# Performance work log

Measured on AMD Instinct MI355X. Metric: run time of the kernel, lower is better.

## Reference

```python
import jax, jax.numpy as jnp
import numpy as np
import math


def _attn(q, k, v):
    # q,k,v: [B, S, d] (d == 1 here). bmm -> scale -> softmax -> bmm.
    scale = 1.0 / math.sqrt(q.shape[2])
    e = jnp.einsum('bsd,btd->bst', q, k) * scale  # [B, S, S]
    w = jax.nn.softmax(e, axis=2)
    return jnp.einsum('bst,btd->bsd', w, v)


def setup_inputs() -> dict:
    key = jax.random.key(0)
    ks = jax.random.split(key, 12)
    B, D = 32, 768
    CLF_OUT = 7
    inp = {}
    names = ['sentence', 'target_spkr_snts', 'other_spkr_snts', 'scene_desc', 'scene_sent']
    for i, name in enumerate(names):
        inp[name] = jax.random.normal(ks[i], (B, D), dtype=jnp.float32)
    inp['W_shared'] = jax.random.normal(ks[5], (768, 512), dtype=jnp.float32) * 0.02
    inp['b_shared'] = jnp.zeros((512,), dtype=jnp.float32)
    inp['W1'] = jax.random.normal(ks[6], (3840, 256), dtype=jnp.float32) * 0.02
    inp['b1'] = jnp.zeros((256,), dtype=jnp.float32)
    inp['W2'] = jax.random.normal(ks[7], (256, CLF_OUT), dtype=jnp.float32) * 0.02
    inp['b2'] = jnp.zeros((CLF_OUT,), dtype=jnp.float32)
    return inp


def reference(sentence, target_spkr_snts, other_spkr_snts, scene_desc, scene_sent,
              W_shared, b_shared, W1, b1, W2, b2):
    B = sentence.shape[0]
    s = sentence[..., None]             # [B, 768, 1]
    sd = scene_desc[..., None]
    ts = target_spkr_snts[..., None]
    oth = other_spkr_snts[..., None]
    ss = scene_sent[..., None]

    speaker_context = _attn(oth, ts, ts)   # [B, 768, 1]
    scene_context = _attn(ss, ss, sd)      # [B, 768, 1]

    sentence_shared = sentence @ W_shared + b_shared                     # [B, 512]
    scene_context_shared = scene_context.reshape(B, -1) @ W_shared + b_shared
    speaker_context_shared = speaker_context.reshape(B, -1) @ W_shared + b_shared

    fused = jnp.concatenate([s, scene_context, speaker_context], axis=1)  # [B, 2304, 1]
    z = _attn(fused, fused, fused)                                        # [B, 2304, 1]

    final = jnp.concatenate([z.reshape(B, -1), sentence_shared,
                             scene_context_shared, speaker_context_shared], axis=1)  # [B, 3840]
    h = jax.nn.relu(final @ W1 + b1)   # dropout is identity in eval mode
    return jax.nn.sigmoid(h @ W2 + b2)  # [B, 7]
```

## Files before the change

### kernel.cpp

```cpp
#include <hip/hip_runtime.h>
#include <math.h>

#define LOG2E 1.44269504088896340736f
typedef float v2f __attribute__((ext_vector_type(2)));


__device__ __forceinline__ void proj_512(
    const float* __restrict__ xsrc,
    const float* __restrict__ Ws,
    const float* __restrict__ bs,
    float* __restrict__ dst,
    float* xb,
    float (*red)[512],
    int tid)
{
    if (tid < 512) { xb[tid] = xsrc[tid]; }
    if (tid >= 256) { xb[tid + 256] = xsrc[tid + 256]; }
    __syncthreads();

    const int g = tid >> 7;
    const int q = tid & 127;
    const float4* __restrict__ Wv = (const float4*)Ws;
    float ax = 0.f, ay = 0.f, az = 0.f, aw = 0.f;
    #pragma unroll 8
    for (int k = g; k < 768; k += 4) {
        const float xv = xb[k];
        const float4 w = Wv[k * 128 + q];
        ax += xv * w.x; ay += xv * w.y; az += xv * w.z; aw += xv * w.w;
    }
    red[g][q * 4 + 0] = ax;
    red[g][q * 4 + 1] = ay;
    red[g][q * 4 + 2] = az;
    red[g][q * 4 + 3] = aw;
    __syncthreads();

    if (tid < 512) {
        dst[tid] = bs[tid] + red[0][tid] + red[1][tid] + red[2][tid] + red[3][tid];
    }
}

__global__ __launch_bounds__(512) void k1_small_attn_proj0(
    const float* __restrict__ sentence,
    const float* __restrict__ target,
    const float* __restrict__ other,
    const float* __restrict__ scene_desc,
    const float* __restrict__ scene_sent,
    const float* __restrict__ Ws,
    const float* __restrict__ bs,
    float* __restrict__ ctx,
    float* __restrict__ final_)
{
    const int b = blockIdx.x;
    const int y = blockIdx.y;
    const int tid = threadIdx.x;
    __shared__ float s0[768];
    __shared__ float s1[768];
    __shared__ float red[4][512];

    if (y < 12) {
        const int part = y / 6;
        const int rg = y - part * 6;
        const float* qp; const float* kp; const float* vp;
        if (part == 0) { qp = scene_sent + b * 768; kp = qp;               vp = scene_desc + b * 768; }
        else           { qp = other + b * 768;      kp = target + b * 768; vp = kp; }
        for (int i = tid; i < 768; i += 512) { s0[i] = kp[i]; s1[i] = vp[i]; }
        __syncthreads();

        const int r0  = rg * 128 + (tid >> 3);
        const int r1  = r0 + 64;
        const int sub = tid & 7;
        const float qA = qp[r0] * LOG2E;
        const float qB = qp[r1] * LOG2E;
        const v2f qA2 = {qA, qA}, qB2 = {qB, qB};
        const float4* __restrict__ kv = (const float4*)s0;
        const float4* __restrict__ vv = (const float4*)s1;
        v2f nA0 = {0.f,0.f}, nA1 = {0.f,0.f}, dA0 = {0.f,0.f}, dA1 = {0.f,0.f};
        v2f nB0 = {0.f,0.f}, nB1 = {0.f,0.f}, dB0 = {0.f,0.f}, dB1 = {0.f,0.f};
        #pragma unroll 4
        for (int i = 0; i < 24; ++i) {
            const int j = sub + 8 * i;
            const float4 k4 = kv[j];
            const float4 v4 = vv[j];
            const v2f ka = {k4.x, k4.y}, kb = {k4.z, k4.w};
            const v2f va = {v4.x, v4.y}, vb2 = {v4.z, v4.w};
            const v2f xaA = qA2 * ka, xbA = qA2 * kb;
            const v2f eaA = {__builtin_amdgcn_exp2f(xaA.x), __builtin_amdgcn_exp2f(xaA.y)};
            const v2f ebA = {__builtin_amdgcn_exp2f(xbA.x), __builtin_amdgcn_exp2f(xbA.y)};
            nA0 += eaA * va;  dA0 += eaA;
            nA1 += ebA * vb2; dA1 += ebA;
            const v2f xaB = qB2 * ka, xbB = qB2 * kb;
            const v2f eaB = {__builtin_amdgcn_exp2f(xaB.x), __builtin_amdgcn_exp2f(xaB.y)};
            const v2f ebB = {__builtin_amdgcn_exp2f(xbB.x), __builtin_amdgcn_exp2f(xbB.y)};
            nB0 += eaB * va;  dB0 += eaB;
            nB1 += ebB * vb2; dB1 += ebB;
        }
        float numA = (nA0.x + nA0.y) + (nA1.x + nA1.y);
        float denA = (dA0.x + dA0.y) + (dA1.x + dA1.y);
        float numB = (nB0.x + nB0.y) + (nB1.x + nB1.y);
        float denB = (dB0.x + dB0.y) + (dB1.x + dB1.y);
        numA += __shfl_xor(numA, 1, 64); numA += __shfl_xor(numA, 2, 64); numA += __shfl_xor(numA, 4, 64);
        denA += __shfl_xor(denA, 1, 64); denA += __shfl_xor(denA, 2, 64); denA += __shfl_xor(denA, 4, 64);
        numB += __shfl_xor(numB, 1, 64); numB += __shfl_xor(numB, 2, 64); numB += __shfl_xor(numB, 4, 64);
        denB += __shfl_xor(denB, 1, 64); denB += __shfl_xor(denB, 2, 64); denB += __shfl_xor(denB, 4, 64);
        if (sub == 0) {
            ctx[b * 1536 + part * 768 + r0] = numA / denA;
            ctx[b * 1536 + part * 768 + r1] = numB / denB;
        }
    } else {
        proj_512(sentence + b * 768, Ws, bs, final_ + b * 3840 + 2304, s0, red, tid);
    }
}

__global__ __launch_bounds__(512) void k2_fused_attn_proj12(
    const float* __restrict__ sentence,
    const float* __restrict__ ctx,
    const float* __restrict__ Ws,
    const float* __restrict__ bs,
    float* __restrict__ final_)
{
    const int b = blockIdx.x;
    const int y = blockIdx.y;
    const int tid = threadIdx.x;
    __shared__ float vb[2304];
    __shared__ float red[4][512];

    if (y < 18) {
        for (int i = tid; i < 2304; i += 512)
            vb[i] = (i < 768) ? sentence[b * 768 + i] : ctx[b * 1536 + (i - 768)];
        __syncthreads();

        const int r0  = y * 128 + (tid >> 3);
        const int r1  = r0 + 64;
        const int sub = tid & 7;
        const float qA = vb[r0] * LOG2E;
        const float qB = vb[r1] * LOG2E;
        const v2f qA2 = {qA, qA}, qB2 = {qB, qB};
        const float4* __restrict__ fv = (const float4*)vb;
        v2f nA0 = {0.f,0.f}, nA1 = {0.f,0.f}, dA0 = {0.f,0.f}, dA1 = {0.f,0.f};
        v2f nB0 = {0.f,0.f}, nB1 = {0.f,0.f}, dB0 = {0.f,0.f}, dB1 = {0.f,0.f};
        #pragma unroll 4
        for (int i = 0; i < 72; ++i) {
            const int j = sub + 8 * i;
            const float4 f4 = fv[j];
            const v2f fa = {f4.x, f4.y}, fb = {f4.z, f4.w};
            const v2f xaA = qA2 * fa, xbA = qA2 * fb;
            const v2f eaA = {__builtin_amdgcn_exp2f(xaA.x), __builtin_amdgcn_exp2f(xaA.y)};
            const v2f ebA = {__builtin_amdgcn_exp2f(xbA.x), __builtin_amdgcn_exp2f(xbA.y)};
            nA0 += eaA * fa; dA0 += eaA;
            nA1 += ebA * fb; dA1 += ebA;
            const v2f xaB = qB2 * fa, xbB = qB2 * fb;
            const v2f eaB = {__builtin_amdgcn_exp2f(xaB.x), __builtin_amdgcn_exp2f(xaB.y)};
            const v2f ebB = {__builtin_amdgcn_exp2f(xbB.x), __builtin_amdgcn_exp2f(xbB.y)};
            nB0 += eaB * fa; dB0 += eaB;
            nB1 += ebB * fb; dB1 += ebB;
        }
        float numA = (nA0.x + nA0.y) + (nA1.x + nA1.y);
        float denA = (dA0.x + dA0.y) + (dA1.x + dA1.y);
        float numB = (nB0.x + nB0.y) + (nB1.x + nB1.y);
        float denB = (dB0.x + dB0.y) + (dB1.x + dB1.y);
        numA += __shfl_xor(numA, 1, 64); numA += __shfl_xor(numA, 2, 64); numA += __shfl_xor(numA, 4, 64);
        denA += __shfl_xor(denA, 1, 64); denA += __shfl_xor(denA, 2, 64); denA += __shfl_xor(denA, 4, 64);
        numB += __shfl_xor(numB, 1, 64); numB += __shfl_xor(numB, 2, 64); numB += __shfl_xor(numB, 4, 64);
        denB += __shfl_xor(denB, 1, 64); denB += __shfl_xor(denB, 2, 64); denB += __shfl_xor(denB, 4, 64);
        if (sub == 0) {
            final_[b * 3840 + r0] = numA / denA;
            final_[b * 3840 + r1] = numB / denB;
        }
    } else {
        const int p = y - 17;
        proj_512(ctx + b * 1536 + (p - 1) * 768, Ws, bs,
                 final_ + b * 3840 + 2304 + p * 512, vb, red, tid);
    }
}

__global__ __launch_bounds__(1024) void mlp_part_kernel(
    const float* __restrict__ final_,
    const float* __restrict__ W1,
    float* __restrict__ hpart)
{
    const int b = blockIdx.x;
    const int c = blockIdx.y;
    const int tid = threadIdx.x;
    const int base = c * 480;

    __shared__ float fb[480];
    __shared__ float red[16][256];
    if (tid < 480) fb[tid] = final_[b * 3840 + base + tid];
    __syncthreads();

    const int g = tid >> 6;
    const int q = tid & 63;
    const float4* __restrict__ Wv = (const float4*)W1;
    float ax = 0.f, ay = 0.f, az = 0.f, aw = 0.f;
    const int l0 = g * 30;
    #pragma unroll 5
    for (int kk = 0; kk < 30; ++kk) {
        const float xv = fb[l0 + kk];
        const float4 w = Wv[(base + l0 + kk) * 64 + q];
        ax += xv * w.x; ay += xv * w.y; az += xv * w.z; aw += xv * w.w;
    }
    red[g][q * 4 + 0] = ax;
    red[g][q * 4 + 1] = ay;
    red[g][q * 4 + 2] = az;
    red[g][q * 4 + 3] = aw;
    __syncthreads();

    if (tid < 256) {
        float s = 0.f;
        #pragma unroll
        for (int g2 = 0; g2 < 16; ++g2) s += red[g2][tid];
        hpart[(b * 8 + c) * 256 + tid] = s;
    }
}

__global__ __launch_bounds__(512) void mlp_tail_kernel(
    const float* __restrict__ hpart,
    const float* __restrict__ b1,
    const float* __restrict__ W2,
    const float* __restrict__ b2,
    float* __restrict__ out)
{
    const int b = blockIdx.x;
    const int tid = threadIdx.x;

    __shared__ float hb[256];
    if (tid < 256) {
        float s = b1[tid];
        #pragma unroll
        for (int c = 0; c < 8; ++c) s += hpart[(b * 8 + c) * 256 + tid];
        hb[tid] = fmaxf(s, 0.f);
    }
    __syncthreads();

    const int w = tid >> 6;
    const int lane = tid & 63;
    if (w < 7) {
        float a = 0.f;
        #pragma unroll
        for (int c = lane; c < 256; c += 64)
            a += hb[c] * W2[c * 7 + w];
        #pragma unroll
        for (int off = 32; off > 0; off >>= 1)
            a += __shfl_down(a, off, 64);
        if (lane == 0)
            out[b * 7 + w] = 1.f / (1.f + __expf(-(a + b2[w])));
    }
}

extern "C" void kernel_launch(void* const* d_in, const int* in_sizes, int n_in,
                              void* d_out, int out_size, void* d_ws, size_t ws_size,
                              hipStream_t stream) {
    const float* sentence   = (const float*)d_in[0];
    const float* target     = (const float*)d_in[1];
    const float* other      = (const float*)d_in[2];
    const float* scene_desc = (const float*)d_in[3];
    const float* scene_sent = (const float*)d_in[4];
    const float* Ws         = (const float*)d_in[5];
    const float* bs         = (const float*)d_in[6];
    const float* W1         = (const float*)d_in[7];
    const float* b1         = (const float*)d_in[8];
    const float* W2         = (const float*)d_in[9];
    const float* b2         = (const float*)d_in[10];
    float* out = (float*)d_out;

    float* ctx    = (float*)d_ws;
    float* final_ = ctx + 32 * 1536;
    float* hpart  = final_ + 32 * 3840;

    k1_small_attn_proj0<<<dim3(32, 13), 512, 0, stream>>>(sentence, target, other,
                                                          scene_desc, scene_sent,
                                                          Ws, bs, ctx, final_);
    k2_fused_attn_proj12<<<dim3(32, 20), 512, 0, stream>>>(sentence, ctx, Ws, bs, final_);
    mlp_part_kernel<<<dim3(32, 8), 1024, 0, stream>>>(final_, W1, hpart);
    mlp_tail_kernel<<<32, 512, 0, stream>>>(hpart, b1, W2, b2, out);
}
```

Baseline: 58.22 us.

## Merge four kernels into one cooperative persistent kernel with grid syncs

Replaces the four separate launches (small attention plus projection, fused attention plus projections, MLP partial, MLP tail) with a single cooperative kernel. Blocks loop over work items per phase and use grid.sync between phases. The MLP partial stage is also split into 16 chunks of 240 rows instead of 8 of 480. This targets launch overhead and inter-kernel gaps, but adds grid-wide barrier cost and an occupancy query on the host every call.

New measurement: 164.8 us. 183% more time.

```diff
diff --git a/kernel.cpp b/kernel.cpp
--- a/kernel.cpp
+++ b/kernel.cpp
@@ -1,17 +1,20 @@
 #include <hip/hip_runtime.h>
+#include <hip/hip_cooperative_groups.h>
 #include <math.h>
+
+namespace cg = cooperative_groups;
 
 #define LOG2E 1.44269504088896340736f
 typedef float v2f __attribute__((ext_vector_type(2)));
 
 
-__device__ __forceinline__ void proj_512(
+__device__ __forceinline__ void proj_768x512(
     const float* __restrict__ xsrc,
     const float* __restrict__ Ws,
     const float* __restrict__ bs,
     float* __restrict__ dst,
     float* xb,
-    float (*red)[512],
+    float* redf,
     int tid)
 {
     if (tid < 512) { xb[tid] = xsrc[tid]; }
@@ -28,18 +31,67 @@
         const float4 w = Wv[k * 128 + q];
         ax += xv * w.x; ay += xv * w.y; az += xv * w.z; aw += xv * w.w;
     }
-    red[g][q * 4 + 0] = ax;
-    red[g][q * 4 + 1] = ay;
-    red[g][q * 4 + 2] = az;
-    red[g][q * 4 + 3] = aw;
+    redf[g * 512 + q * 4 + 0] = ax;
+    redf[g * 512 + q * 4 + 1] = ay;
+    redf[g * 512 + q * 4 + 2] = az;
+    redf[g * 512 + q * 4 + 3] = aw;
     __syncthreads();
 
     if (tid < 512) {
-        dst[tid] = bs[tid] + red[0][tid] + red[1][tid] + red[2][tid] + red[3][tid];
-    }
-}
-
-__global__ __launch_bounds__(512) void k1_small_attn_proj0(
+        dst[tid] = bs[tid] + redf[0 * 512 + tid] + redf[1 * 512 + tid]
+                           + redf[2 * 512 + tid] + redf[3 * 512 + tid];
+    }
+}
+
+__device__ __forceinline__ void attn128(
+    const float* __restrict__ qsrc,
+    const float4* __restrict__ kv,
+    const float4* __restrict__ vv,
+    int n4,
+    int r0base, int tid,
+    float* __restrict__ out0,
+    int outstride_r0)
+{
+    const int r0  = r0base + (tid >> 3);
+    const int r1  = r0 + 64;
+    const int sub = tid & 7;
+    const float qA = qsrc[r0] * LOG2E;
+    const float qB = qsrc[r1] * LOG2E;
+    const v2f qA2 = {qA, qA}, qB2 = {qB, qB};
+    v2f nA0 = {0.f,0.f}, nA1 = {0.f,0.f}, dA0 = {0.f,0.f}, dA1 = {0.f,0.f};
+    v2f nB0 = {0.f,0.f}, nB1 = {0.f,0.f}, dB0 = {0.f,0.f}, dB1 = {0.f,0.f};
+    #pragma unroll 4
+    for (int j = sub; j < n4; j += 8) {
+        const float4 k4 = kv[j];
+        const float4 v4 = vv[j];
+        const v2f ka = {k4.x, k4.y}, kb = {k4.z, k4.w};
+        const v2f va = {v4.x, v4.y}, vb2 = {v4.z, v4.w};
+        const v2f xaA = qA2 * ka, xbA = qA2 * kb;
+        const v2f eaA = {__builtin_amdgcn_exp2f(xaA.x), __builtin_amdgcn_exp2f(xaA.y)};
+        const v2f ebA = {__builtin_amdgcn_exp2f(xbA.x), __builtin_amdgcn_exp2f(xbA.y)};
+        nA0 += eaA * va;  dA0 += eaA;
+        nA1 += ebA * vb2; dA1 += ebA;
+        const v2f xaB = qB2 * ka, xbB = qB2 * kb;
+        const v2f eaB = {__builtin_amdgcn_exp2f(xaB.x), __builtin_amdgcn_exp2f(xaB.y)};
+        const v2f ebB = {__builtin_amdgcn_exp2f(xbB.x), __builtin_amdgcn_exp2f(xbB.y)};
+        nB0 += eaB * va;  dB0 += eaB;
+        nB1 += ebB * vb2; dB1 += ebB;
+    }
+    float numA = (nA0.x + nA0.y) + (nA1.x + nA1.y);
+    float denA = (dA0.x + dA0.y) + (dA1.x + dA1.y);
+    float numB = (nB0.x + nB0.y) + (nB1.x + nB1.y);
+    float denB = (dB0.x + dB0.y) + (dB1.x + dB1.y);
+    numA += __shfl_xor(numA, 1, 64); numA += __shfl_xor(numA, 2, 64); numA += __shfl_xor(numA, 4, 64);
+    denA += __shfl_xor(denA, 1, 64); denA += __shfl_xor(denA, 2, 64); denA += __shfl_xor(denA, 4, 64);
+    numB += __shfl_xor(numB, 1, 64); numB += __shfl_xor(numB, 2, 64); numB += __shfl_xor(numB, 4, 64);
+    denB += __shfl_xor(denB, 1, 64); denB += __shfl_xor(denB, 2, 64); denB += __shfl_xor(denB, 4, 64);
+    if (sub == 0) {
+        out0[outstride_r0 + r0 - r0base] = numA / denA;
+        out0[outstride_r0 + r1 - r0base] = numB / denB;
+    }
+}
+
+__global__ __launch_bounds__(512) void mega_kernel(
     const float* __restrict__ sentence,
     const float* __restrict__ target,
     const float* __restrict__ other,
@@ -47,203 +99,120 @@
     const float* __restrict__ scene_sent,
     const float* __restrict__ Ws,
     const float* __restrict__ bs,
-    float* __restrict__ ctx,
-    float* __restrict__ final_)
-{
-    const int b = blockIdx.x;
-    const int y = blockIdx.y;
-    const int tid = threadIdx.x;
-    __shared__ float s0[768];
-    __shared__ float s1[768];
-    __shared__ float red[4][512];
-
-    if (y < 12) {
-        const int part = y / 6;
-        const int rg = y - part * 6;
-        const float* qp; const float* kp; const float* vp;
-        if (part == 0) { qp = scene_sent + b * 768; kp = qp;               vp = scene_desc + b * 768; }
-        else           { qp = other + b * 768;      kp = target + b * 768; vp = kp; }
-        for (int i = tid; i < 768; i += 512) { s0[i] = kp[i]; s1[i] = vp[i]; }
-        __syncthreads();
-
-        const int r0  = rg * 128 + (tid >> 3);
-        const int r1  = r0 + 64;
-        const int sub = tid & 7;
-        const float qA = qp[r0] * LOG2E;
-        const float qB = qp[r1] * LOG2E;
-        const v2f qA2 = {qA, qA}, qB2 = {qB, qB};
-        const float4* __restrict__ kv = (const float4*)s0;
-        const float4* __restrict__ vv = (const float4*)s1;
-        v2f nA0 = {0.f,0.f}, nA1 = {0.f,0.f}, dA0 = {0.f,0.f}, dA1 = {0.f,0.f};
-        v2f nB0 = {0.f,0.f}, nB1 = {0.f,0.f}, dB0 = {0.f,0.f}, dB1 = {0.f,0.f};
-        #pragma unroll 4
-        for (int i = 0; i < 24; ++i) {
-            const int j = sub + 8 * i;
-            const float4 k4 = kv[j];
-            const float4 v4 = vv[j];
-            const v2f ka = {k4.x, k4.y}, kb = {k4.z, k4.w};
-            const v2f va = {v4.x, v4.y}, vb2 = {v4.z, v4.w};
-            const v2f xaA = qA2 * ka, xbA = qA2 * kb;
-            const v2f eaA = {__builtin_amdgcn_exp2f(xaA.x), __builtin_amdgcn_exp2f(xaA.y)};
-            const v2f ebA = {__builtin_amdgcn_exp2f(xbA.x), __builtin_amdgcn_exp2f(xbA.y)};
-            nA0 += eaA * va;  dA0 += eaA;
-            nA1 += ebA * vb2; dA1 += ebA;
-            const v2f xaB = qB2 * ka, xbB = qB2 * kb;
-            const v2f eaB = {__builtin_amdgcn_exp2f(xaB.x), __builtin_amdgcn_exp2f(xaB.y)};
-            const v2f ebB = {__builtin_amdgcn_exp2f(xbB.x), __builtin_amdgcn_exp2f(xbB.y)};
-            nB0 += eaB * va;  dB0 += eaB;
-            nB1 += ebB * vb2; dB1 += ebB;
-        }
-        float numA = (nA0.x + nA0.y) + (nA1.x + nA1.y);
-        float denA = (dA0.x + dA0.y) + (dA1.x + dA1.y);
-        float numB = (nB0.x + nB0.y) + (nB1.x + nB1.y);
-        float denB = (dB0.x + dB0.y) + (dB1.x + dB1.y);
-        numA += __shfl_xor(numA, 1, 64); numA += __shfl_xor(numA, 2, 64); numA += __shfl_xor(numA, 4, 64);
-        denA += __shfl_xor(denA, 1, 64); denA += __shfl_xor(denA, 2, 64); denA += __shfl_xor(denA, 4, 64);
-        numB += __shfl_xor(numB, 1, 64); numB += __shfl_xor(numB, 2, 64); numB += __shfl_xor(numB, 4, 64);
-        denB += __shfl_xor(denB, 1, 64); denB += __shfl_xor(denB, 2, 64); denB += __shfl_xor(denB, 4, 64);
-        if (sub == 0) {
-            ctx[b * 1536 + part * 768 + r0] = numA / denA;
-            ctx[b * 1536 + part * 768 + r1] = numB / denB;
-        }
-    } else {
-        proj_512(sentence + b * 768, Ws, bs, final_ + b * 3840 + 2304, s0, red, tid);
-    }
-}
-
-__global__ __launch_bounds__(512) void k2_fused_attn_proj12(
-    const float* __restrict__ sentence,
-    const float* __restrict__ ctx,
-    const float* __restrict__ Ws,
-    const float* __restrict__ bs,
-    float* __restrict__ final_)
-{
-    const int b = blockIdx.x;
-    const int y = blockIdx.y;
-    const int tid = threadIdx.x;
-    __shared__ float vb[2304];
-    __shared__ float red[4][512];
-
-    if (y < 18) {
-        for (int i = tid; i < 2304; i += 512)
-            vb[i] = (i < 768) ? sentence[b * 768 + i] : ctx[b * 1536 + (i - 768)];
-        __syncthreads();
-
-        const int r0  = y * 128 + (tid >> 3);
-        const int r1  = r0 + 64;
-        const int sub = tid & 7;
-        const float qA = vb[r0] * LOG2E;
-        const float qB = vb[r1] * LOG2E;
-        const v2f qA2 = {qA, qA}, qB2 = {qB, qB};
-        const float4* __restrict__ fv = (const float4*)vb;
-        v2f nA0 = {0.f,0.f}, nA1 = {0.f,0.f}, dA0 = {0.f,0.f}, dA1 = {0.f,0.f};
-        v2f nB0 = {0.f,0.f}, nB1 = {0.f,0.f}, dB0 = {0.f,0.f}, dB1 = {0.f,0.f};
-        #pragma unroll 4
-        for (int i = 0; i < 72; ++i) {
-            const int j = sub + 8 * i;
-            const float4 f4 = fv[j];
-            const v2f fa = {f4.x, f4.y}, fb = {f4.z, f4.w};
-            const v2f xaA = qA2 * fa, xbA = qA2 * fb;
-            const v2f eaA = {__builtin_amdgcn_exp2f(xaA.x), __builtin_amdgcn_exp2f(xaA.y)};
-            const v2f ebA = {__builtin_amdgcn_exp2f(xbA.x), __builtin_amdgcn_exp2f(xbA.y)};
-            nA0 += eaA * fa; dA0 += eaA;
-            nA1 += ebA * fb; dA1 += ebA;
-            const v2f xaB = qB2 * fa, xbB = qB2 * fb;
-            const v2f eaB = {__builtin_amdgcn_exp2f(xaB.x), __builtin_amdgcn_exp2f(xaB.y)};
-            const v2f ebB = {__builtin_amdgcn_exp2f(xbB.x), __builtin_amdgcn_exp2f(xbB.y)};
-            nB0 += eaB * fa; dB0 += eaB;
-            nB1 += ebB * fb; dB1 += ebB;
-        }
-        float numA = (nA0.x + nA0.y) + (nA1.x + nA1.y);
-        float denA = (dA0.x + dA0.y) + (dA1.x + dA1.y);
-        float numB = (nB0.x + nB0.y) + (nB1.x + nB1.y);
-        float denB = (dB0.x + dB0.y) + (dB1.x + dB1.y);
-        numA += __shfl_xor(numA, 1, 64); numA += __shfl_xor(numA, 2, 64); numA += __shfl_xor(numA, 4, 64);
-        denA += __shfl_xor(denA, 1, 64); denA += __shfl_xor(denA, 2, 64); denA += __shfl_xor(denA, 4, 64);
-        numB += __shfl_xor(numB, 1, 64); numB += __shfl_xor(numB, 2, 64); numB += __shfl_xor(numB, 4, 64);
-        denB += __shfl_xor(denB, 1, 64); denB += __shfl_xor(denB, 2, 64); denB += __shfl_xor(denB, 4, 64);
-        if (sub == 0) {
-            final_[b * 3840 + r0] = numA / denA;
-            final_[b * 3840 + r1] = numB / denB;
-        }
-    } else {
-        const int p = y - 17;
-        proj_512(ctx + b * 1536 + (p - 1) * 768, Ws, bs,
-                 final_ + b * 3840 + 2304 + p * 512, vb, red, tid);
-    }
-}
-
-__global__ __launch_bounds__(1024) void mlp_part_kernel(
-    const float* __restrict__ final_,
     const float* __restrict__ W1,
-    float* __restrict__ hpart)
-{
-    const int b = blockIdx.x;
-    const int c = blockIdx.y;
-    const int tid = threadIdx.x;
-    const int base = c * 480;
-
-    __shared__ float fb[480];
-    __shared__ float red[16][256];
-    if (tid < 480) fb[tid] = final_[b * 3840 + base + tid];
-    __syncthreads();
-
-    const int g = tid >> 6;
-    const int q = tid & 63;
-    const float4* __restrict__ Wv = (const float4*)W1;
-    float ax = 0.f, ay = 0.f, az = 0.f, aw = 0.f;
-    const int l0 = g * 30;
-    #pragma unroll 5
-    for (int kk = 0; kk < 30; ++kk) {
-        const float xv = fb[l0 + kk];
-        const float4 w = Wv[(base + l0 + kk) * 64 + q];
-        ax += xv * w.x; ay += xv * w.y; az += xv * w.z; aw += xv * w.w;
-    }
-    red[g][q * 4 + 0] = ax;
-    red[g][q * 4 + 1] = ay;
-    red[g][q * 4 + 2] = az;
-    red[g][q * 4 + 3] = aw;
-    __syncthreads();
-
-    if (tid < 256) {
-        float s = 0.f;
-        #pragma unroll
-        for (int g2 = 0; g2 < 16; ++g2) s += red[g2][tid];
-        hpart[(b * 8 + c) * 256 + tid] = s;
-    }
-}
-
-__global__ __launch_bounds__(512) void mlp_tail_kernel(
-    const float* __restrict__ hpart,
     const float* __restrict__ b1,
     const float* __restrict__ W2,
     const float* __restrict__ b2,
-    float* __restrict__ out)
+    float* __restrict__ out,
+    float* __restrict__ ctx,
+    float* __restrict__ final_,
+    float* __restrict__ hpart)
 {
-    const int b = blockIdx.x;
+    cg::grid_group grid = cg::this_grid();
     const int tid = threadIdx.x;
-
-    __shared__ float hb[256];
-    if (tid < 256) {
-        float s = b1[tid];
-        #pragma unroll
-        for (int c = 0; c < 8; ++c) s += hpart[(b * 8 + c) * 256 + tid];
-        hb[tid] = fmaxf(s, 0.f);
-    }
-    __syncthreads();
-
-    const int w = tid >> 6;
-    const int lane = tid & 63;
-    if (w < 7) {
-        float a = 0.f;
-        #pragma unroll
-        for (int c = lane; c < 256; c += 64)
-            a += hb[c] * W2[c * 7 + w];
-        #pragma unroll
-        for (int off = 32; off > 0; off >>= 1)
-            a += __shfl_down(a, off, 64);
-        if (lane == 0)
-            out[b * 7 + w] = 1.f / (1.f + __expf(-(a + b2[w])));
+    __shared__ float smem[2304];
+    __shared__ float redf[2048];
+
+    for (int item = blockIdx.x; item < 416; item += gridDim.x) {
+        __syncthreads();
+        if (item < 384) {
+            const int b    = item / 12;
+            const int rem  = item - b * 12;
+            const int part = rem / 6;
+            const int rg   = rem - part * 6;
+            const float* qp; const float* kp; const float* vp;
+            if (part == 0) { qp = scene_sent + b * 768; kp = qp;               vp = scene_desc + b * 768; }
+            else           { qp = other + b * 768;      kp = target + b * 768; vp = kp; }
+            for (int i = tid; i < 768; i += 512) { smem[i] = kp[i]; smem[768 + i] = vp[i]; }
+            __syncthreads();
+            attn128(qp, (const float4*)smem, (const float4*)(smem + 768), 192,
+                    rg * 128, tid, ctx + b * 1536 + part * 768 + rg * 128, 0);
+        } else {
+            const int b = item - 384;
+            proj_768x512(sentence + b * 768, Ws, bs, final_ + b * 3840 + 2304,
+                         smem, redf, tid);
+        }
+    }
+    grid.sync();
+
+    for (int item = blockIdx.x; item < 640; item += gridDim.x) {
+        __syncthreads();
+        if (item < 576) {
+            const int b = item / 18;
+            const int y = item - b * 18;
+            for (int i = tid; i < 2304; i += 512)
+                smem[i] = (i < 768) ? sentence[b * 768 + i] : ctx[b * 1536 + (i - 768)];
+            __syncthreads();
+            attn128(smem, (const float4*)smem, (const float4*)smem, 576,
+                    y * 128, tid, final_ + b * 3840 + y * 128, 0);
+        } else {
+            const int j = item - 576;
+            const int b = j >> 1;
+            const int p = 1 + (j & 1);
+            proj_768x512(ctx + b * 1536 + (p - 1) * 768, Ws, bs,
+                         final_ + b * 3840 + 2304 + p * 512, smem, redf, tid);
+        }
+    }
+    grid.sync();
+
+    for (int item = blockIdx.x; item < 512; item += gridDim.x) {
+        __syncthreads();
+        const int b = item >> 4;
+        const int c = item & 15;
+        const int base = c * 240;
+        if (tid < 240) smem[tid] = final_[b * 3840 + base + tid];
+        __syncthreads();
+
+        const int g = tid >> 6;
+        const int q = tid & 63;
+        const float4* __restrict__ Wv = (const float4*)W1;
+        float ax = 0.f, ay = 0.f, az = 0.f, aw = 0.f;
+        const int l0 = g * 30;
+        #pragma unroll 5
+        for (int kk = 0; kk < 30; ++kk) {
+            const float xv = smem[l0 + kk];
+            const float4 w = Wv[(base + l0 + kk) * 64 + q];
+            ax += xv * w.x; ay += xv * w.y; az += xv * w.z; aw += xv * w.w;
+        }
+        redf[g * 256 + q * 4 + 0] = ax;
+        redf[g * 256 + q * 4 + 1] = ay;
+        redf[g * 256 + q * 4 + 2] = az;
+        redf[g * 256 + q * 4 + 3] = aw;
+        __syncthreads();
+
+        if (tid < 256) {
+            float s = 0.f;
+            #pragma unroll
+            for (int g2 = 0; g2 < 8; ++g2) s += redf[g2 * 256 + tid];
+            hpart[(b * 16 + c) * 256 + tid] = s;
+        }
+    }
+    grid.sync();
+
+    for (int item = blockIdx.x; item < 32; item += gridDim.x) {
+        __syncthreads();
+        const int b = item;
+        if (tid < 256) {
+            float s = b1[tid];
+            #pragma unroll
+            for (int c = 0; c < 16; ++c) s += hpart[(b * 16 + c) * 256 + tid];
+            smem[tid] = fmaxf(s, 0.f);
+        }
+        __syncthreads();
+
+        const int w = tid >> 6;
+        const int lane = tid & 63;
+        if (w < 7) {
+            float a = 0.f;
+            #pragma unroll
+            for (int c = lane; c < 256; c += 64)
+                a += smem[c] * W2[c * 7 + w];
+            #pragma unroll
+            for (int off = 32; off > 0; off >>= 1)
+                a += __shfl_down(a, off, 64);
+            if (lane == 0)
+                out[b * 7 + w] = 1.f / (1.f + __expf(-(a + b2[w])));
+        }
     }
 }
 
@@ -267,10 +236,18 @@
     float* final_ = ctx + 32 * 1536;
     float* hpart  = final_ + 32 * 3840;
 
-    k1_small_attn_proj0<<<dim3(32, 13), 512, 0, stream>>>(sentence, target, other,
-                                                          scene_desc, scene_sent,
-                                                          Ws, bs, ctx, final_);
-    k2_fused_attn_proj12<<<dim3(32, 20), 512, 0, stream>>>(sentence, ctx, Ws, bs, final_);
-    mlp_part_kernel<<<dim3(32, 8), 1024, 0, stream>>>(final_, W1, hpart);
-    mlp_tail_kernel<<<32, 512, 0, stream>>>(hpart, b1, W2, b2, out);
-}
+    int nb = 0;
+    (void)hipOccupancyMaxActiveBlocksPerMultiprocessor(&nb, mega_kernel, 512, 0);
+    if (nb < 1) nb = 1;
+    int gridSize = nb * 256;
+    if (gridSize > 640) gridSize = 640;
+
+    void* args[] = {
+        (void*)&sentence, (void*)&target, (void*)&other, (void*)&scene_desc,
+        (void*)&scene_sent, (void*)&Ws, (void*)&bs, (void*)&W1, (void*)&b1,
+        (void*)&W2, (void*)&b2, (void*)&out, (void*)&ctx, (void*)&final_,
+        (void*)&hpart
+    };
+    (void)hipLaunchCooperativeKernel((void*)mega_kernel, dim3(gridSize), dim3(512),
+                                     args, 0, stream);
+}
```
